# Optimization experiments

Measured on AMD Instinct MI355X. Metric: run time of the kernel, lower is better.

Reference implementation:

```python
import jax, jax.numpy as jnp
import numpy as np

ANGLE_BITS = 3          # TurboQuantConfig.angle_bits default
LEVELS = 2 ** ANGLE_BITS
PI = np.pi


def _angle_ranges(d_minus_1, dtype):
    # hyperspherical coords: first d-2 angles in [0, pi], last angle in [0, 2*pi)
    return jnp.concatenate([
        jnp.full((d_minus_1 - 1,), PI, dtype),
        jnp.full((1,), 2.0 * PI, dtype),
    ])


def polar_compress(x):
    """x: [..., d] -> (r [...,1], theta_indices int32 [..., d-1])."""
    # suffix norms s_i = ||x[i:]|| via reversed cumsum of squares
    suffix = jnp.sqrt(jnp.cumsum((x * x)[..., ::-1], axis=-1)[..., ::-1])
    r = suffix[..., :1]
    cos_t = jnp.clip(x[..., :-1] / jnp.maximum(suffix[..., :-1], 1e-12), -1.0, 1.0)
    theta = jnp.arccos(cos_t)                      # [..., d-1], in [0, pi]
    # last angle carries the sign of x[..., -1]: map to [0, 2*pi)
    last = jnp.where(x[..., -1:] < 0, 2.0 * PI - theta[..., -1:], theta[..., -1:])
    theta = jnp.concatenate([theta[..., :-1], last], axis=-1)
    ranges = _angle_ranges(theta.shape[-1], theta.dtype)
    idx = jnp.round(theta / ranges * (LEVELS - 1)).astype(jnp.int32)
    return r, idx


def polar_decompress(r, idx):
    """(r [...,1], idx [..., d-1]) -> x_hat [..., d] via trig products."""
    d1 = idx.shape[-1]
    ranges = _angle_ranges(d1, r.dtype)
    theta = idx.astype(r.dtype) / (LEVELS - 1) * ranges
    sinp = jnp.cumprod(jnp.sin(theta), axis=-1)                 # [..., d-1]
    prods = jnp.concatenate([jnp.ones_like(r), sinp], axis=-1)  # [..., d]
    coss = jnp.concatenate([jnp.cos(theta), jnp.ones_like(r)], axis=-1)
    return r * prods * coss


def setup_inputs() -> dict:
    key = jax.random.key(0)
    kq, kk, kv, kn = jax.random.split(key, 4)
    B, H, T, k, d = 1, 32, 8192, 16, 128
    return {
        "queries": jax.random.normal(kq, (B, H, k, d), jnp.float32),
        "keys": jax.random.normal(kk, (B, H, T, d), jnp.float32),
        "values": jax.random.normal(kv, (B, H, T, d), jnp.float32),
        # faithful stand-in for `torch.randn_like(scores) * 0.01` QJL correction,
        # materialized deterministically as an input
        "qjl_noise": jax.random.normal(kn, (B, H, k, T), jnp.float32) * 0.01,
    }


def reference(queries, keys, values, qjl_noise):
    d = queries.shape[-1]
    # compress_kv_cache: polar angle quantization of keys and values
    r_k, idx_k = polar_compress(keys)
    r_v, idx_v = polar_compress(values)
    # compute_attention_with_compressed_kv: decompress-then-attend
    keys_polar = polar_decompress(r_k, idx_k)      # [B,H,T,d]
    values_polar = polar_decompress(r_v, idx_v)    # [B,H,T,d]
    scores = jnp.einsum('bhkd,bhtd->bhkt', queries, keys_polar) / jnp.sqrt(
        jnp.asarray(d, queries.dtype))
    scores = scores + qjl_noise
    attn = jax.nn.softmax(scores, axis=-1)
    return jnp.einsum('bhkt,bhtd->bhkd', attn, values_polar)
```

## Files before the change

### kernel.cpp

```cpp
#include <hip/hip_runtime.h>
#include <math.h>

typedef __attribute__((ext_vector_type(8))) short bf16x8;
typedef __attribute__((ext_vector_type(4))) float f32x4;
typedef __attribute__((ext_vector_type(2))) float f32x2;

#define HEADS 32
#define SEQT  8192
#define DIM   128
#define NQ    16
#define BPH   64
#define BTOK  128
#define WTOK  32
#define CHK   16
#define NPART BPH
#define PSTR  132
#define QPAD  136
#define QSCALE 0.08838834764831845f

#define OFF_QS    0
#define OFF_PS    4352
#define OFF_ML    8448
#define OFF_RAW   8960
#define OFF_KS    41728
#define OFF_MERGE 8960
#define LDS_BYTES 59136

#define W1SQ 0.9504844339512096f
#define W2SQ 0.6112604669781572f
#define W3SQ 0.1882550990706332f
#define S1C  0.4338837391175581f
#define S2C  0.7818314824680298f
#define S3C  0.9749279121818236f
#define C1C  0.9009688679024191f
#define C2C  0.6234898018587336f
#define C3C  0.2225209339563144f
#define B1SQ 0.8117449009293667f
#define B2SQ 0.0495155660487913f
#define B3SQ 0.3887395330218429f

#define DPP_QP_XOR1 0xB1
#define DPP_QP_XOR2 0x4E
#define DPP_QP_SHL1 0x39
#define DPP_QP_SHR1 0x90
#define DPP_QP_SHR2 0x44
#define DPP_QP_BC0  0x00
#define DPP_QP_BC3  0xFF
#define DPP_HALF_MIRR 0x141
#define DPP_MIRR      0x140

template <int CTRL>
__device__ __forceinline__ float dpp0(float v) {
  return __int_as_float(__builtin_amdgcn_update_dpp(
      0, __float_as_int(v), CTRL, 0xF, 0xF, true));
}
__device__ __forceinline__ float rmax16(float v) {
  v = fmaxf(v, dpp0<DPP_QP_XOR1>(v));
  v = fmaxf(v, dpp0<DPP_QP_XOR2>(v));
  v = fmaxf(v, dpp0<DPP_HALF_MIRR>(v));
  v = fmaxf(v, dpp0<DPP_MIRR>(v));
  return v;
}
__device__ __forceinline__ float rsum16(float v) {
  v += dpp0<DPP_QP_XOR1>(v);
  v += dpp0<DPP_QP_XOR2>(v);
  v += dpp0<DPP_HALF_MIRR>(v);
  v += dpp0<DPP_MIRR>(v);
  return v;
}
__device__ __forceinline__ float rdlane(float v, int l) {
  return __int_as_float(__builtin_amdgcn_readlane(__float_as_int(v), l));
}
__device__ __forceinline__ unsigned short f2bf(float f) {
  unsigned u = __float_as_uint(f);
  u += 0x7FFFu + ((u >> 16) & 1u);
  return (unsigned short)(u >> 16);
}
__device__ __forceinline__ unsigned cvtpk(float lo, float hi) {
  unsigned r;
  asm("v_cvt_pk_bf16_f32 %0, %1, %2" : "=v"(r) : "v"(lo), "v"(hi));
  return r;
}

__device__ __forceinline__ void stage16(const float* __restrict__ g, char* lds, int lane) {
  const int h2 = lane >> 5;
  const int qs = (lane >> 3) & 3;
  const int js = lane & 7;
#pragma unroll
  for (int i = 0; i < 8; ++i) {
    const int t = 2 * i + h2;
    const int sb = js ^ (t & 7);
    __builtin_amdgcn_global_load_lds(
        (const float*)(g + (size_t)t * DIM + qs * 32 + sb * 4),
        (float*)(lds + i * 1024), 16, 0, 0);
  }
}

template <bool KOUT>
__device__ __forceinline__ void decomp8(
    const float* __restrict__ rawW, int sc, int lane,
    unsigned short* __restrict__ KsW, float* __restrict__ VsW,
    const float* __restrict__ nextsrc, char* __restrict__ rawBytes)
{
  const int tloc = lane >> 3;
  const int o    = lane & 7;
  const int T    = sc * 8 + tloc;

  float x[16];
#pragma unroll
  for (int j = 0; j < 4; ++j) {
    const int s = ((o >> 1) << 3) | ((((o & 1) << 2) | j) ^ tloc);
    const float4 v = *(const float4*)(rawW + T * 128 + 4 * s);
    x[4*j+0] = v.x; x[4*j+1] = v.y; x[4*j+2] = v.z; x[4*j+3] = v.w;
  }
  float qa0 = 0.f, qa1 = 0.f;
#pragma unroll
  for (int i = 0; i < 16; i += 2) {
    qa0 = fmaf(x[i], x[i], qa0);
    qa1 = fmaf(x[i+1], x[i+1], qa1);
  }
  const float qs = qa0 + qa1;
  const float a1 = dpp0<DPP_QP_SHL1>(qs);
  const float t1 = qs + (((lane & 3) == 3) ? 0.f : a1);
  const float b1 = dpp0<DPP_QP_XOR2>(t1);
  const float t2 = t1 + (((lane & 3) < 2) ? b1 : 0.f);
  const float qt = dpp0<DPP_QP_BC0>(t2);
  const float ot = dpp0<DPP_HALF_MIRR>(qt);
  const float total = qt + ot;
  const float S = t2 + ((o < 4) ? ot : 0.f);

  if (nextsrc) {
    __builtin_amdgcn_sched_barrier(0);
    stage16(nextsrc, nextsrc ? rawBytes : rawBytes, lane);
  }

  const float r = sqrtf(total);

  float run = S, psin = 1.f, run14 = 0.f;
  float sv[16], cv[16];
#pragma unroll
  for (int i = 0; i < 16; ++i) {
    const float u = x[i] * x[i];
    if (i == 14) run14 = run;
    const bool lo2 = u < W2SQ * run;
    const float thr = lo2 ? W3SQ : W1SQ;
    const bool bx = u < thr * run;
    const float ssin = lo2 ? (bx ? S3C : S2C) : (bx ? S1C : 0.f);
    float scos = lo2 ? (bx ? C3C : C2C) : (bx ? C1C : 1.f);
    scos = copysignf(scos, x[i]);
    sv[i] = ssin; cv[i] = scos;
    psin *= ssin;
    run -= u;
  }
  const float p1 = dpp0<DPP_QP_SHR1>(psin);
  const float e1 = psin * (((lane & 3) == 0) ? 1.f : p1);
  const float p2 = dpp0<DPP_QP_SHR2>(e1);
  const float e2 = e1 * (((lane & 3) < 2) ? 1.f : p2);
  const float pq = dpp0<DPP_QP_BC3>(e2);
  const float po = dpp0<DPP_HALF_MIRR>(pq);
  const float e3 = e2 * ((o >= 4) ? po : 1.f);
  const float sh = dpp0<DPP_QP_SHR1>(e3);
  const float E = ((lane & 3) == 0) ? ((o < 4) ? 1.f : po) : sh;

  float rcum = r * E;
  unsigned short* krow = KsW + T * QPAD + o * 16;
  float* vrow = VsW + tloc * 132 + o * 16;
#pragma unroll
  for (int g = 0; g < 2; ++g) {
    float outv[8];
    float rc14 = rcum;
#pragma unroll
    for (int k = 0; k < 8; ++k) {
      const int i = 8 * g + k;
      if (i == 14) rc14 = rcum;
      outv[k] = rcum * cv[i];
      rcum *= sv[i];
    }
    if (g == 1) {
      const float u14 = x[14] * x[14];
      const bool neg = x[14] < 0.f;
      const bool cc1 = u14 < B1SQ * run14;
      const bool cc2 = u14 < B2SQ * run14;
      const bool cc3 = u14 > B3SQ * run14;
      const float cpos = cc2 ? -C3C : (cc1 ? C2C : 1.f);
      const float spos = cc2 ? S3C : (cc1 ? S2C : 0.f);
      const float cneg = cc3 ? -C1C : -C3C;
      const float sneg = cc3 ? S1C : S3C;
      const float cB = neg ? cneg : cpos;
      float sB = neg ? sneg : spos;
      sB = copysignf(sB, x[15]);
      const bool o7 = (o == 7);
      outv[6] = o7 ? rc14 * cB : outv[6];
      outv[7] = o7 ? rc14 * sB : outv[7];
    }
    if (KOUT) {
      uint4 w;
      w.x = cvtpk(outv[0], outv[1]);
      w.y = cvtpk(outv[2], outv[3]);
      w.z = cvtpk(outv[4], outv[5]);
      w.w = cvtpk(outv[6], outv[7]);
      *(uint4*)&krow[8 * g] = w;
    } else {
      *(float4*)&vrow[8 * g]     = make_float4(outv[0], outv[1], outv[2], outv[3]);
      *(float4*)&vrow[8 * g + 4] = make_float4(outv[4], outv[5], outv[6], outv[7]);
    }
  }
}

__global__ __launch_bounds__(256, 2)
void attn_partial(const float* __restrict__ Q, const float* __restrict__ K,
                  const float* __restrict__ V, const float* __restrict__ noise,
                  float* __restrict__ part) {
  __shared__ __align__(16) char RAW[LDS_BYTES];
  unsigned short* Qs = (unsigned short*)(RAW + OFF_QS);
  float*          Ps = (float*)(RAW + OFF_PS);
  float2*         Ml = (float2*)(RAW + OFF_ML);

  const int tid  = threadIdx.x;
  const int lane = tid & 63;
  const int wv   = tid >> 6;
  const int h    = blockIdx.x / BPH;
  const int bh   = blockIdx.x % BPH;
  const int r16  = lane & 15, G = lane >> 4;

  char* rawB = RAW + OFF_RAW + wv * 8192;
  const float* rawW = (const float*)rawB;
  unsigned short* KsW = (unsigned short*)(RAW + OFF_KS + wv * 4352);
  float* VsW = (float*)KsW;
  float* myP = Ps + wv * (CHK * NQ);

  const size_t hoff = (size_t)h * SEQT * DIM;
  const int t0 = bh * BTOK + wv * WTOK;
  const float* Kg = K + hoff + (size_t)t0 * DIM;
  const float* Vg = V + hoff + (size_t)t0 * DIM;

  stage16(Kg, rawB, lane);
  {
    const float* Qh = Q + (size_t)h * NQ * DIM;
    for (int i = tid; i < NQ * DIM; i += 256)
      Qs[(i >> 7) * QPAD + (i & 127)] = f2bf(Qh[i] * QSCALE);
  }
  __syncthreads();

  bf16x8 qa[4];
#pragma unroll
  for (int c = 0; c < 4; ++c)
    qa[c] = *(const bf16x8*)&Qs[r16 * QPAD + c * 32 + G * 8];

  f32x2 acc[NQ];
#pragma unroll
  for (int qq = 0; qq < NQ; ++qq) acc[qq] = (f32x2){0.f, 0.f};
  float m_r[4] = {-INFINITY, -INFINITY, -INFINITY, -INFINITY};
  float l_r[4] = {0.f, 0.f, 0.f, 0.f};

  const float* nh = noise + (size_t)h * NQ * SEQT + t0 + r16;

#pragma unroll 1
  for (int ch = 0; ch < 2; ++ch) {
    asm volatile("s_waitcnt vmcnt(0)" ::: "memory");

    const float* Vsrc = Vg + (size_t)ch * CHK * DIM;
#pragma unroll 1
    for (int sc = 0; sc < 2; ++sc)
      decomp8<true>(rawW, sc, lane, KsW, VsW, (sc == 1) ? Vsrc : nullptr, rawB);

    f32x4 d0 = {0.f, 0.f, 0.f, 0.f};
#pragma unroll
    for (int c = 0; c < 4; ++c) {
      bf16x8 b0 = *(const bf16x8*)&KsW[r16 * QPAD + c * 32 + G * 8];
      d0 = __builtin_amdgcn_mfma_f32_16x16x32_bf16(qa[c], b0, d0, 0, 0, 0);
    }
    const float* nt = nh + ch * CHK;
    float s0_[4];
#pragma unroll
    for (int rr = 0; rr < 4; ++rr)
      s0_[rr] = d0[rr] + nt[(size_t)(4 * G + rr) * SEQT];
    float al_r[4];
#pragma unroll
    for (int rr = 0; rr < 4; ++rr) {
      float mt = rmax16(s0_[rr]);
      float mn = fmaxf(m_r[rr], mt);
      al_r[rr] = __expf(m_r[rr] - mn);
      m_r[rr] = mn;
    }
    float p0[4];
#pragma unroll
    for (int rr = 0; rr < 4; ++rr) {
      p0[rr] = __expf(s0_[rr] - m_r[rr]);
      l_r[rr] = l_r[rr] * al_r[rr] + rsum16(p0[rr]);
    }
    *(float4*)&myP[r16 * NQ + 4 * G] = make_float4(p0[0], p0[1], p0[2], p0[3]);
#pragma unroll
    for (int qq = 0; qq < NQ; ++qq) {
      float alq = rdlane(al_r[qq & 3], (qq >> 2) << 4);
      acc[qq] *= (f32x2){alq, alq};
    }

    asm volatile("s_waitcnt vmcnt(0)" ::: "memory");

    const float* Knext = (ch == 0) ? (Kg + CHK * DIM) : nullptr;
#pragma unroll 1
    for (int sc = 0; sc < 2; ++sc) {
      decomp8<false>(rawW, sc, lane, KsW, VsW, (sc == 1) ? Knext : nullptr, rawB);
#pragma unroll 2
      for (int tt = 0; tt < 8; ++tt) {
        float2 vh = *(const float2*)&VsW[tt * 132 + 2 * lane];
        f32x2 vh2 = {vh.x, vh.y};
        const float* pv = &myP[(sc * 8 + tt) * NQ];
        float4 pa = ((const float4*)pv)[0];
        float4 pb = ((const float4*)pv)[1];
        float4 pc = ((const float4*)pv)[2];
        float4 pd = ((const float4*)pv)[3];
        float pq[NQ] = {pa.x, pa.y, pa.z, pa.w, pb.x, pb.y, pb.z, pb.w,
                        pc.x, pc.y, pc.z, pc.w, pd.x, pd.y, pd.z, pd.w};
#pragma unroll
        for (int qq = 0; qq < NQ; ++qq)
          acc[qq] = __builtin_elementwise_fma((f32x2){pq[qq], pq[qq]}, vh2, acc[qq]);
      }
    }
  }

  if (r16 == 0) {
#pragma unroll
    for (int rr = 0; rr < 4; ++rr)
      Ml[wv * NQ + 4 * G + rr] = make_float2(m_r[rr], l_r[rr]);
  }
  __syncthreads();
#pragma unroll
  for (int qq = 0; qq < NQ; ++qq) {
    float2 e0 = Ml[0 * NQ + qq], e1 = Ml[1 * NQ + qq];
    float2 e2 = Ml[2 * NQ + qq], e3 = Ml[3 * NQ + qq];
    float Mq = fmaxf(fmaxf(e0.x, e1.x), fmaxf(e2.x, e3.x));
    float own = (wv == 0) ? e0.x : ((wv == 1) ? e1.x : ((wv == 2) ? e2.x : e3.x));
    float al = __expf(own - Mq);
    acc[qq] *= (f32x2){al, al};
  }
  float* buf = (float*)(RAW + OFF_MERGE);
  if (wv >= 2) {
#pragma unroll
    for (int qq = 0; qq < NQ; ++qq)
      *(float2*)&buf[(wv - 2) * 2048 + qq * 128 + 2 * lane] =
          make_float2(acc[qq].x, acc[qq].y);
  }
  __syncthreads();
  if (wv < 2) {
#pragma unroll
    for (int qq = 0; qq < NQ; ++qq) {
      float2 t = *(const float2*)&buf[wv * 2048 + qq * 128 + 2 * lane];
      acc[qq] += (f32x2){t.x, t.y};
    }
  }
  __syncthreads();
  if (wv == 1) {
#pragma unroll
    for (int qq = 0; qq < NQ; ++qq)
      *(float2*)&buf[qq * 128 + 2 * lane] = make_float2(acc[qq].x, acc[qq].y);
  }
  __syncthreads();
  if (wv == 0) {
    float* P = part + ((size_t)h * NPART + bh) * (NQ * PSTR);
#pragma unroll
    for (int qq = 0; qq < NQ; ++qq) {
      float2 t = *(const float2*)&buf[qq * 128 + 2 * lane];
      *(float2*)&P[qq * PSTR + 4 + 2 * lane] =
          make_float2(acc[qq].x + t.x, acc[qq].y + t.y);
      float2 e0 = Ml[0 * NQ + qq], e1 = Ml[1 * NQ + qq];
      float2 e2 = Ml[2 * NQ + qq], e3 = Ml[3 * NQ + qq];
      float Mq = fmaxf(fmaxf(e0.x, e1.x), fmaxf(e2.x, e3.x));
      float Lq = e0.y * __expf(e0.x - Mq) + e1.y * __expf(e1.x - Mq) +
                 e2.y * __expf(e2.x - Mq) + e3.y * __expf(e3.x - Mq);
      if (lane == 0) *(float2*)&P[qq * PSTR] = make_float2(Mq, Lq);
    }
  }
}

__global__ __launch_bounds__(128)
void attn_reduce(const float* __restrict__ part, float* __restrict__ out) {
  __shared__ float wgt[NPART];
  __shared__ float Lsh;
  const int tid = threadIdx.x;
  const int h = blockIdx.x >> 4;
  const int q = blockIdx.x & 15;
  const float* P = part + (size_t)h * NPART * NQ * PSTR;
  if (tid < NPART) {
    float2 ml = *(const float2*)&P[((size_t)tid * NQ + q) * PSTR];
    float M = ml.x;
#pragma unroll
    for (int off = 1; off < 64; off <<= 1)
      M = fmaxf(M, __shfl_xor(M, off, 64));
    float w = __expf(ml.x - M);
    wgt[tid] = w;
    float L = ml.y * w;
#pragma unroll
    for (int off = 1; off < 64; off <<= 1)
      L += __shfl_xor(L, off, 64);
    if (tid == 0) Lsh = L;
  }
  __syncthreads();
  const float* A = P + (size_t)q * PSTR + 4 + tid;
  float o = 0.f;
#pragma unroll 8
  for (int c = 0; c < NPART; ++c)
    o = fmaf(wgt[c], A[(size_t)c * NQ * PSTR], o);
  out[((size_t)h * NQ + q) * DIM + tid] = o * (1.0f / Lsh);
}

extern "C" void kernel_launch(void* const* d_in, const int* in_sizes, int n_in,
                              void* d_out, int out_size, void* d_ws, size_t ws_size,
                              hipStream_t stream) {
  (void)in_sizes; (void)n_in; (void)out_size; (void)ws_size;
  const float* Q = (const float*)d_in[0];
  const float* K = (const float*)d_in[1];
  const float* V = (const float*)d_in[2];
  const float* noise = (const float*)d_in[3];
  float* part = (float*)d_ws;
  attn_partial<<<dim3(HEADS * BPH), dim3(256), 0, stream>>>(Q, K, V, noise, part);
  attn_reduce<<<dim3(HEADS * NQ), dim3(128), 0, stream>>>(part, (float*)d_out);
}
```

Measured before the change: 310.3 us.

## Halve staging buffers, swizzle LDS tiles, and raise occupancy to four blocks

Shrinks the per-wave raw staging buffer from 16 to 8 tokens, which cuts LDS from about 59 KB to 40 KB and lets launch bounds rise from 2 to 4 blocks per CU. The padded K/V/Q LDS rows are replaced with XOR swizzles to avoid bank conflicts without padding. The prefetch of the next 8-token tile now issues right after the raw data is read into registers. This adds more wait points and a finer-grained pipeline, and the tighter register budget may cause spills.

```diff
diff --git a/kernel.cpp b/kernel.cpp
--- a/kernel.cpp
+++ b/kernel.cpp
@@ -15,16 +15,15 @@
 #define CHK   16
 #define NPART BPH
 #define PSTR  132
-#define QPAD  136
 #define QSCALE 0.08838834764831845f
 
 #define OFF_QS    0
-#define OFF_PS    4352
-#define OFF_ML    8448
-#define OFF_RAW   8960
-#define OFF_KS    41728
-#define OFF_MERGE 8960
-#define LDS_BYTES 59136
+#define OFF_PS    4096
+#define OFF_RAW   8192
+#define OFF_KS    24576
+#define OFF_ML    0
+#define OFF_MERGE 8192
+#define LDS_BYTES 40960
 
 #define W1SQ 0.9504844339512096f
 #define W2SQ 0.6112604669781572f
@@ -49,6 +48,8 @@
 #define DPP_HALF_MIRR 0x141
 #define DPP_MIRR      0x140
 
+#define WAITV asm volatile("s_waitcnt vmcnt(0)" ::: "memory")
+
 template <int CTRL>
 __device__ __forceinline__ float dpp0(float v) {
   return __int_as_float(__builtin_amdgcn_update_dpp(
@@ -82,14 +83,14 @@
   return r;
 }
 
-__device__ __forceinline__ void stage16(const float* __restrict__ g, char* lds, int lane) {
+__device__ __forceinline__ void stage8(const float* __restrict__ g, char* lds, int lane) {
   const int h2 = lane >> 5;
   const int qs = (lane >> 3) & 3;
   const int js = lane & 7;
 #pragma unroll
-  for (int i = 0; i < 8; ++i) {
+  for (int i = 0; i < 4; ++i) {
     const int t = 2 * i + h2;
-    const int sb = js ^ (t & 7);
+    const int sb = js ^ t;
     __builtin_amdgcn_global_load_lds(
         (const float*)(g + (size_t)t * DIM + qs * 32 + sb * 4),
         (float*)(lds + i * 1024), 16, 0, 0);
@@ -98,21 +99,25 @@
 
 template <bool KOUT>
 __device__ __forceinline__ void decomp8(
-    const float* __restrict__ rawW, int sc, int lane,
-    unsigned short* __restrict__ KsW, float* __restrict__ VsW,
-    const float* __restrict__ nextsrc, char* __restrict__ rawBytes)
+    const float* rawW, int lane,
+    unsigned short* KsW, float* VsW, int q8,
+    const float* nextsrc, char* rawBytes)
 {
   const int tloc = lane >> 3;
   const int o    = lane & 7;
-  const int T    = sc * 8 + tloc;
 
   float x[16];
 #pragma unroll
   for (int j = 0; j < 4; ++j) {
     const int s = ((o >> 1) << 3) | ((((o & 1) << 2) | j) ^ tloc);
-    const float4 v = *(const float4*)(rawW + T * 128 + 4 * s);
+    const float4 v = *(const float4*)(rawW + tloc * 128 + 4 * s);
     x[4*j+0] = v.x; x[4*j+1] = v.y; x[4*j+2] = v.z; x[4*j+3] = v.w;
   }
+  asm volatile("s_waitcnt lgkmcnt(0)" ::: "memory");
+  __builtin_amdgcn_sched_barrier(0);
+  if (nextsrc) stage8(nextsrc, rawBytes, lane);
+  __builtin_amdgcn_sched_barrier(0);
+
   float qa0 = 0.f, qa1 = 0.f;
 #pragma unroll
   for (int i = 0; i < 16; i += 2) {
@@ -128,11 +133,6 @@
   const float ot = dpp0<DPP_HALF_MIRR>(qt);
   const float total = qt + ot;
   const float S = t2 + ((o < 4) ? ot : 0.f);
-
-  if (nextsrc) {
-    __builtin_amdgcn_sched_barrier(0);
-    stage16(nextsrc, nextsrc ? rawBytes : rawBytes, lane);
-  }
 
   const float r = sqrtf(total);
 
@@ -163,8 +163,7 @@
   const float E = ((lane & 3) == 0) ? ((o < 4) ? 1.f : po) : sh;
 
   float rcum = r * E;
-  unsigned short* krow = KsW + T * QPAD + o * 16;
-  float* vrow = VsW + tloc * 132 + o * 16;
+  const int T = q8 * 8 + tloc;
 #pragma unroll
   for (int g = 0; g < 2; ++g) {
     float outv[8];
@@ -199,15 +198,16 @@
       w.y = cvtpk(outv[2], outv[3]);
       w.z = cvtpk(outv[4], outv[5]);
       w.w = cvtpk(outv[6], outv[7]);
-      *(uint4*)&krow[8 * g] = w;
+      *(uint4*)&KsW[T * 128 + ((o * 16 + 8 * g) ^ (tloc << 3))] = w;
     } else {
-      *(float4*)&vrow[8 * g]     = make_float4(outv[0], outv[1], outv[2], outv[3]);
-      *(float4*)&vrow[8 * g + 4] = make_float4(outv[4], outv[5], outv[6], outv[7]);
-    }
-  }
-}
-
-__global__ __launch_bounds__(256, 2)
+      const int f0 = (o * 16 + 8 * g) ^ (tloc << 2);
+      *(float4*)&VsW[tloc * 128 + f0]       = make_float4(outv[0], outv[1], outv[2], outv[3]);
+      *(float4*)&VsW[tloc * 128 + (f0 ^ 4)] = make_float4(outv[4], outv[5], outv[6], outv[7]);
+    }
+  }
+}
+
+__global__ __launch_bounds__(256, 4)
 void attn_partial(const float* __restrict__ Q, const float* __restrict__ K,
                   const float* __restrict__ V, const float* __restrict__ noise,
                   float* __restrict__ part) {
@@ -223,9 +223,9 @@
   const int bh   = blockIdx.x % BPH;
   const int r16  = lane & 15, G = lane >> 4;
 
-  char* rawB = RAW + OFF_RAW + wv * 8192;
+  char* rawB = RAW + OFF_RAW + wv * 4096;
   const float* rawW = (const float*)rawB;
-  unsigned short* KsW = (unsigned short*)(RAW + OFF_KS + wv * 4352);
+  unsigned short* KsW = (unsigned short*)(RAW + OFF_KS + wv * 4096);
   float* VsW = (float*)KsW;
   float* myP = Ps + wv * (CHK * NQ);
 
@@ -234,18 +234,18 @@
   const float* Kg = K + hoff + (size_t)t0 * DIM;
   const float* Vg = V + hoff + (size_t)t0 * DIM;
 
-  stage16(Kg, rawB, lane);
+  stage8(Kg, rawB, lane);
   {
     const float* Qh = Q + (size_t)h * NQ * DIM;
     for (int i = tid; i < NQ * DIM; i += 256)
-      Qs[(i >> 7) * QPAD + (i & 127)] = f2bf(Qh[i] * QSCALE);
+      Qs[i] = f2bf(Qh[i] * QSCALE);
   }
   __syncthreads();
 
   bf16x8 qa[4];
 #pragma unroll
   for (int c = 0; c < 4; ++c)
-    qa[c] = *(const bf16x8*)&Qs[r16 * QPAD + c * 32 + G * 8];
+    qa[c] = *(const bf16x8*)&Qs[r16 * 128 + c * 32 + G * 8];
 
   f32x2 acc[NQ];
 #pragma unroll
@@ -257,17 +257,18 @@
 
 #pragma unroll 1
   for (int ch = 0; ch < 2; ++ch) {
-    asm volatile("s_waitcnt vmcnt(0)" ::: "memory");
-
-    const float* Vsrc = Vg + (size_t)ch * CHK * DIM;
-#pragma unroll 1
-    for (int sc = 0; sc < 2; ++sc)
-      decomp8<true>(rawW, sc, lane, KsW, VsW, (sc == 1) ? Vsrc : nullptr, rawB);
+    const float* KgC = Kg + ch * 2048;
+    const float* VgC = Vg + ch * 2048;
+
+    WAITV;
+    decomp8<true>(rawW, lane, KsW, VsW, 0, KgC + 1024, rawB);
+    WAITV;
+    decomp8<true>(rawW, lane, KsW, VsW, 1, VgC, rawB);
 
     f32x4 d0 = {0.f, 0.f, 0.f, 0.f};
 #pragma unroll
     for (int c = 0; c < 4; ++c) {
-      bf16x8 b0 = *(const bf16x8*)&KsW[r16 * QPAD + c * 32 + G * 8];
+      bf16x8 b0 = *(const bf16x8*)&KsW[r16 * 128 + ((c * 32 + G * 8) ^ ((r16 & 7) << 3))];
       d0 = __builtin_amdgcn_mfma_f32_16x16x32_bf16(qa[c], b0, d0, 0, 0, 0);
     }
     const float* nt = nh + ch * CHK;
@@ -296,15 +297,15 @@
       acc[qq] *= (f32x2){alq, alq};
     }
 
-    asm volatile("s_waitcnt vmcnt(0)" ::: "memory");
-
-    const float* Knext = (ch == 0) ? (Kg + CHK * DIM) : nullptr;
 #pragma unroll 1
     for (int sc = 0; sc < 2; ++sc) {
-      decomp8<false>(rawW, sc, lane, KsW, VsW, (sc == 1) ? Knext : nullptr, rawB);
+      const float* nxt = (sc == 0) ? (VgC + 1024)
+                                   : ((ch == 0) ? (KgC + 2048) : nullptr);
+      WAITV;
+      decomp8<false>(rawW, lane, KsW, VsW, 0, nxt, rawB);
 #pragma unroll 2
       for (int tt = 0; tt < 8; ++tt) {
-        float2 vh = *(const float2*)&VsW[tt * 132 + 2 * lane];
+        float2 vh = *(const float2*)&VsW[tt * 128 + ((2 * lane) ^ (tt << 2))];
         f32x2 vh2 = {vh.x, vh.y};
         const float* pv = &myP[(sc * 8 + tt) * NQ];
         float4 pa = ((const float4*)pv)[0];
```

New measurement: 344.2 us. +10.9%, slower.
